# Kernel tuning notes

Measured on AMD Instinct MI355X. Metric: run time of the kernel, lower is better.

The kernel has to match this reference:

```python
import jax, jax.numpy as jnp
import numpy as np

T = 131072          # total characters across all words/sentences
N_WORDS = 32768
WORD_DIM = 1024
CHAR_DIM = 256
HIDDEN = 512
NUM_EMB = 40


def setup_inputs() -> dict:
    key = jax.random.key(0)
    ks = jax.random.split(key, 9)
    return {
        "word_emb": jax.random.normal(ks[0], (N_WORDS, WORD_DIM), jnp.float32),
        "char_ids": jax.random.randint(ks[1], (T,), 0, NUM_EMB, jnp.int32),
        "word_ids": jax.random.randint(ks[2], (T,), 0, N_WORDS, jnp.int32),
        "E": jax.random.normal(ks[3], (NUM_EMB, CHAR_DIM), jnp.float32),
        "W_ih": jax.random.normal(ks[4], (4 * HIDDEN, CHAR_DIM), jnp.float32) * 0.05,
        "b_ih": jax.random.normal(ks[5], (4 * HIDDEN,), jnp.float32) * 0.05,
        "b_hh": jax.random.normal(ks[6], (4 * HIDDEN,), jnp.float32) * 0.05,
        "W_lin": jax.random.normal(ks[7], (WORD_DIM, WORD_DIM + HIDDEN), jnp.float32) * 0.02,
        "b_lin": jax.random.normal(ks[8], (WORD_DIM,), jnp.float32) * 0.02,
    }


def reference(word_emb, char_ids, word_ids, E, W_ih, b_ih, b_hh, W_lin, b_lin):
    # Per-char embedding lookup: [T, CHAR_DIM]
    x = E[char_ids]
    # Single LSTM cell step from zero state (source runs LSTM with seq_len=1,
    # batch=num_chars; h0=c0=0 so W_hh @ h0 vanishes and only b_hh remains).
    gates = x @ W_ih.T + b_ih + b_hh            # [T, 4H], torch gate order i,f,g,o
    i, f, g, o = jnp.split(gates, 4, axis=-1)
    c = jax.nn.sigmoid(i) * jnp.tanh(g)          # f * c0 = 0
    h = jax.nn.sigmoid(o) * jnp.tanh(c)          # [T, HIDDEN]
    # Broadcast each word's embedding to its characters (torch .expand())
    we = word_emb[word_ids]                      # [T, WORD_DIM]
    combined = jnp.concatenate([we, h], axis=-1) # [T, WORD_DIM + HIDDEN]
    return jax.nn.relu(combined @ W_lin.T + b_lin)  # [T, WORD_DIM]
```

## Files before the change

kernel.cpp:

```cpp
#include <hip/hip_runtime.h>
#include <cstdint>
#include <cstddef>

#define T_TOTAL   131072
#define NWORDS    32768
#define WDIM      1024
#define CDIM      256
#define HID       512
#define NEMB      40
#define KDIM      1024
#define NDIM      1024

#define BM 128
#define BN 128
#define BK 32
#define NK (KDIM / BK)
#define EPS 132

#define NCONVB_BLKS (NDIM * KDIM / 4 / 256)
#define NCONVA_BLKS (NWORDS * KDIM / 4 / 256)

typedef __attribute__((ext_vector_type(8))) short bf16x8;
typedef __attribute__((ext_vector_type(4))) float f32x4;
typedef __attribute__((ext_vector_type(4))) unsigned short u16x4;

__device__ __forceinline__ unsigned short f2bf(float x) {
  union { float f; unsigned int u; } v; v.f = x;
  unsigned int r = v.u + 0x7fffu + ((v.u >> 16) & 1u);
  return (unsigned short)(r >> 16);
}
__device__ __forceinline__ float bf2f(unsigned short b) {
  union { float f; unsigned int u; } v; v.u = ((unsigned int)b) << 16;
  return v.f;
}

__device__ __forceinline__ void gld16(const void* src, void* lds) {
  __builtin_amdgcn_global_load_lds(
      (const __attribute__((address_space(1))) unsigned int*)src,
      (__attribute__((address_space(3))) unsigned int*)lds, 16, 0, 0);
}

template <bool DO_A>
__global__ __launch_bounds__(256) void k_prep(
    const float* __restrict__ word_emb, const float* __restrict__ E,
    const float* __restrict__ W_ih, const float* __restrict__ b_ih,
    const float* __restrict__ b_hh, const float* __restrict__ W_lin,
    const float* __restrict__ b_lin,
    unsigned short* __restrict__ Ah,
    unsigned short* __restrict__ Bh, unsigned short* __restrict__ Bl,
    float* __restrict__ Hc) {
  __shared__ float sx[CDIM];
  __shared__ float sh[HID];
  int b = blockIdx.x;
  int tid = threadIdx.x;

  if (b < NEMB) {
    int e = b;
    sx[tid] = E[e * CDIM + tid];
    __syncthreads();
    const float4* xv = (const float4*)sx;
#pragma unroll
    for (int rep = 0; rep < 2; ++rep) {
      int j = rep * 256 + tid;
      float si = b_ih[j] + b_hh[j];
      float sg = b_ih[1024 + j] + b_hh[1024 + j];
      float so = b_ih[1536 + j] + b_hh[1536 + j];
      const float4* wi = (const float4*)&W_ih[(size_t)j * CDIM];
      const float4* wg = (const float4*)&W_ih[(size_t)(1024 + j) * CDIM];
      const float4* wo = (const float4*)&W_ih[(size_t)(1536 + j) * CDIM];
      for (int k = 0; k < CDIM / 4; ++k) {
        float4 d = xv[k];
        float4 a = wi[k]; si += a.x*d.x + a.y*d.y + a.z*d.z + a.w*d.w;
        float4 g = wg[k]; sg += g.x*d.x + g.y*d.y + g.z*d.z + g.w*d.w;
        float4 c = wo[k]; so += c.x*d.x + c.y*d.y + c.z*d.z + c.w*d.w;
      }
      float iv = 1.f / (1.f + expf(-si));
      float cv = iv * tanhf(sg);
      float ov = 1.f / (1.f + expf(-so));
      sh[j] = ov * tanhf(cv);
    }
    __syncthreads();
    const float4* hv = (const float4*)sh;
#pragma unroll
    for (int rep = 0; rep < 4; ++rep) {
      int n = rep * 256 + tid;
      float s = b_lin[n];
      const float4* wl = (const float4*)&W_lin[(size_t)n * 1536 + 1024];
      for (int k = 0; k < HID / 4; ++k) {
        float4 a = wl[k], d = hv[k];
        s += a.x*d.x + a.y*d.y + a.z*d.z + a.w*d.w;
      }
      Hc[e * NDIM + n] = s;
    }
    return;
  }
  b -= NEMB;
  if (b < NCONVB_BLKS) {
    long idx = ((long)b * 256 + tid) * 4;
    long r = idx >> 10;
    int c = (int)(idx & 1023);
    const float4 v = *(const float4*)&W_lin[r * 1536 + c];
    unsigned short h0 = f2bf(v.x), h1 = f2bf(v.y), h2 = f2bf(v.z), h3 = f2bf(v.w);
    u16x4 H = {h0, h1, h2, h3};
    u16x4 L = {f2bf(v.x - bf2f(h0)), f2bf(v.y - bf2f(h1)),
               f2bf(v.z - bf2f(h2)), f2bf(v.w - bf2f(h3))};
    *(u16x4*)&Bh[idx] = H;
    *(u16x4*)&Bl[idx] = L;
    return;
  }
  if (DO_A) {
    b -= NCONVB_BLKS;
    long idx = ((long)b * 256 + tid) * 4;
    const float4 v = *(const float4*)&word_emb[idx];
    u16x4 H = {f2bf(v.x), f2bf(v.y), f2bf(v.z), f2bf(v.w)};
    *(u16x4*)&Ah[idx] = H;
  }
}

template <bool PRECONV>
__global__ __launch_bounds__(256, 3) void k_gemm_p(
    const float* __restrict__ Af,
    const unsigned short* __restrict__ Ah,
    const unsigned short* __restrict__ Bh, const unsigned short* __restrict__ Bl,
    float* __restrict__ P) {
  __shared__ __align__(16) char smem[PRECONV ? 49152 : 65536];

  int nwg = gridDim.x;
  int bid = blockIdx.x;
  int cpx = nwg >> 3;
  int swz = (bid & 7) * cpx + (bid >> 3);
  int bn = swz & 7;
  int bm = swz >> 3;

  int tid = threadIdx.x;
  int lane = tid & 63;
  int w = tid >> 6;
  int wr = w >> 1, wc = w & 1;
  int fr = lane & 15, fq = lane >> 4;

  size_t arow0 = (size_t)bm * BM;
  size_t brow0 = (size_t)bn * BN;

  f32x4 acc[4][4];
#pragma unroll
  for (int i = 0; i < 4; ++i)
#pragma unroll
    for (int j = 0; j < 4; ++j) acc[i][j] = (f32x4)0.0f;

  int bOff[4];
#pragma unroll
  for (int ni = 0; ni < 4; ++ni) {
    int row = wc * 64 + ni * 16 + fr;
    bOff[ni] = row * 64 + ((fq ^ ((row >> 1) & 3)) << 4);
  }
  size_t bS[2]; int bL[2];
#pragma unroll
  for (int is = 0; is < 2; ++is) {
    int off = is * 4096 + tid * 16;
    int r = off >> 6;
    int sp = (off >> 4) & 3;
    int colE = ((sp ^ ((r >> 1) & 3)) << 3);
    bS[is] = (brow0 + r) * KDIM + colE;
    bL[is] = is * 4096 + w * 1024;
  }
  int aOff[4];
#pragma unroll
  for (int mi = 0; mi < 4; ++mi) {
    int row = wr * 64 + mi * 16 + fr;
    aOff[mi] = row * 64 + ((fq ^ ((row >> 1) & 3)) << 4);
  }

  if (PRECONV) {
    size_t aS[2];
#pragma unroll
    for (int is = 0; is < 2; ++is) {
      int off = is * 4096 + tid * 16;
      int r = off >> 6;
      int sp = (off >> 4) & 3;
      int colE = ((sp ^ ((r >> 1) & 3)) << 3);
      aS[is] = (arow0 + r) * KDIM + colE;
    }

    auto STAGE = [&](int buf, int k0) {
      char* b = smem + buf * 24576;
#pragma unroll
      for (int is = 0; is < 2; ++is) {
        gld16(Ah + aS[is] + k0, b + bL[is]);
        gld16(Bh + bS[is] + k0, b + 8192 + bL[is]);
        gld16(Bl + bS[is] + k0, b + 16384 + bL[is]);
      }
    };

    STAGE(0, 0);
    for (int t = 0; t < NK; ++t) {
      char* bufc = smem + (t & 1) * 24576;
      if (t + 1 < NK) {
        STAGE((t + 1) & 1, (t + 1) * BK);
        asm volatile("s_waitcnt vmcnt(6)" ::: "memory");
      } else {
        asm volatile("s_waitcnt vmcnt(0)" ::: "memory");
      }
      __builtin_amdgcn_s_barrier();
      __builtin_amdgcn_sched_barrier(0);

      bf16x8 fah[4], fbh[4], fbl[4];
#pragma unroll
      for (int ni = 0; ni < 4; ++ni) {
        fbh[ni] = *(const bf16x8*)(bufc + 8192 + bOff[ni]);
        fbl[ni] = *(const bf16x8*)(bufc + 16384 + bOff[ni]);
      }
#pragma unroll
      for (int mi = 0; mi < 4; ++mi)
        fah[mi] = *(const bf16x8*)(bufc + aOff[mi]);
      __builtin_amdgcn_s_setprio(1);
#pragma unroll
      for (int mi = 0; mi < 4; ++mi)
#pragma unroll
        for (int ni = 0; ni < 4; ++ni) {
          acc[mi][ni] = __builtin_amdgcn_mfma_f32_16x16x32_bf16(fah[mi], fbh[ni], acc[mi][ni], 0, 0, 0);
          acc[mi][ni] = __builtin_amdgcn_mfma_f32_16x16x32_bf16(fah[mi], fbl[ni], acc[mi][ni], 0, 0, 0);
        }
      __builtin_amdgcn_s_setprio(0);
      __builtin_amdgcn_sched_barrier(0);
      __builtin_amdgcn_s_barrier();
    }
  } else {
    size_t aS[4]; int aL[4];
#pragma unroll
    for (int is = 0; is < 4; ++is) {
      int off = is * 4096 + tid * 16;
      int r = off >> 7;
      int sl = (off >> 4) & 7;
      int col = ((sl ^ (r & 7)) << 2);
      aS[is] = (arow0 + r) * KDIM + col;
      aL[is] = is * 4096 + w * 1024;
    }
    int a1[4], a2[4];
#pragma unroll
    for (int mi = 0; mi < 4; ++mi) {
      int row = wr * 64 + mi * 16 + fr;
      a1[mi] = row * 128 + (((fq << 1)     ^ (row & 7)) << 4);
      a2[mi] = row * 128 + (((fq << 1) + 1) ^ (row & 7)) * 16;
    }

    auto STAGE = [&](int buf, int k0) {
      char* b = smem + buf * 32768;
#pragma unroll
      for (int is = 0; is < 4; ++is) gld16(Af + aS[is] + k0, b + aL[is]);
#pragma unroll
      for (int is = 0; is < 2; ++is) {
        gld16(Bh + bS[is] + k0, b + 16384 + bL[is]);
        gld16(Bl + bS[is] + k0, b + 24576 + bL[is]);
      }
    };

    STAGE(0, 0);
    for (int t = 0; t < NK; ++t) {
      char* bufc = smem + (t & 1) * 32768;
      if (t + 1 < NK) {
        STAGE((t + 1) & 1, (t + 1) * BK);
        asm volatile("s_waitcnt vmcnt(8)" ::: "memory");
      } else {
        asm volatile("s_waitcnt vmcnt(0)" ::: "memory");
      }
      __builtin_amdgcn_s_barrier();
      __builtin_amdgcn_sched_barrier(0);

      bf16x8 fah[4], fbh[4], fbl[4];
#pragma unroll
      for (int ni = 0; ni < 4; ++ni) {
        fbh[ni] = *(const bf16x8*)(bufc + 16384 + bOff[ni]);
        fbl[ni] = *(const bf16x8*)(bufc + 24576 + bOff[ni]);
      }
#pragma unroll
      for (int mi = 0; mi < 4; ++mi) {
        float4 v1 = *(const float4*)(bufc + a1[mi]);
        float4 v2 = *(const float4*)(bufc + a2[mi]);
        union { bf16x8 v; unsigned short u[8]; } H;
        H.u[0] = f2bf(v1.x); H.u[1] = f2bf(v1.y); H.u[2] = f2bf(v1.z); H.u[3] = f2bf(v1.w);
        H.u[4] = f2bf(v2.x); H.u[5] = f2bf(v2.y); H.u[6] = f2bf(v2.z); H.u[7] = f2bf(v2.w);
        fah[mi] = H.v;
      }
      __builtin_amdgcn_s_setprio(1);
#pragma unroll
      for (int mi = 0; mi < 4; ++mi)
#pragma unroll
        for (int ni = 0; ni < 4; ++ni) {
          acc[mi][ni] = __builtin_amdgcn_mfma_f32_16x16x32_bf16(fah[mi], fbh[ni], acc[mi][ni], 0, 0, 0);
          acc[mi][ni] = __builtin_amdgcn_mfma_f32_16x16x32_bf16(fah[mi], fbl[ni], acc[mi][ni], 0, 0, 0);
        }
      __builtin_amdgcn_s_setprio(0);
      __builtin_amdgcn_sched_barrier(0);
      __builtin_amdgcn_s_barrier();
    }
  }

  float* ep = (float*)smem;
  __syncthreads();
#pragma unroll
  for (int half = 0; half < 2; ++half) {
    if (wr == half) {
#pragma unroll
      for (int mi = 0; mi < 4; ++mi)
#pragma unroll
        for (int ni = 0; ni < 4; ++ni)
#pragma unroll
          for (int j = 0; j < 4; ++j) {
            int r = mi * 16 + fq * 4 + j;
            int c = wc * 64 + ni * 16 + fr;
            ep[r * EPS + c] = acc[mi][ni][j];
          }
    }
    __syncthreads();
    for (int i = tid; i < 2048; i += 256) {
      int r = i >> 5;
      int c4 = (i & 31) << 2;
      float4 v = *(const float4*)&ep[r * EPS + c4];
      *(float4*)&P[(arow0 + half * 64 + r) * NDIM + brow0 + c4] = v;
    }
    __syncthreads();
  }
}

__global__ __launch_bounds__(256) void k_out(const int* __restrict__ wid,
                                             const int* __restrict__ cid,
                                             const float* __restrict__ P,
                                             const float* __restrict__ Hc,
                                             float* __restrict__ out) {
  int w = threadIdx.x >> 6, lane = threadIdx.x & 63;
  int t = blockIdx.x * 4 + w;
  int wd = wid[t], cd = cid[t];
  const f32x4* pr = (const f32x4*)&P[(size_t)wd << 10];
  const f32x4* hr = (const f32x4*)&Hc[(size_t)cd << 10];
  f32x4* orow = (f32x4*)&out[(size_t)t << 10];
#pragma unroll
  for (int ch = 0; ch < 4; ++ch) {
    int c = ch * 64 + lane;
    f32x4 a = pr[c];
    f32x4 h4 = hr[c];
    f32x4 r;
    r[0] = fmaxf(a[0] + h4[0], 0.f);
    r[1] = fmaxf(a[1] + h4[1], 0.f);
    r[2] = fmaxf(a[2] + h4[2], 0.f);
    r[3] = fmaxf(a[3] + h4[3], 0.f);
    __builtin_nontemporal_store(r, &orow[c]);
  }
}

extern "C" void kernel_launch(void* const* d_in, const int* in_sizes, int n_in,
                              void* d_out, int out_size, void* d_ws, size_t ws_size,
                              hipStream_t stream) {
  (void)in_sizes; (void)n_in; (void)out_size;
  const float* word_emb = (const float*)d_in[0];
  const int*   char_ids = (const int*)d_in[1];
  const int*   word_ids = (const int*)d_in[2];
  const float* E        = (const float*)d_in[3];
  const float* W_ih     = (const float*)d_in[4];
  const float* b_ih     = (const float*)d_in[5];
  const float* b_hh     = (const float*)d_in[6];
  const float* W_lin    = (const float*)d_in[7];
  const float* b_lin    = (const float*)d_in[8];
  float* out = (float*)d_out;
  char* ws = (char*)d_ws;

  size_t o = 0;
  auto alloc = [&](size_t b) { size_t r = o; o = (o + b + 255) & ~(size_t)255; return r; };
  size_t oHc = alloc((size_t)NEMB * NDIM * 4);
  size_t oBh = alloc((size_t)NDIM * KDIM * 2);
  size_t oBl = alloc((size_t)NDIM * KDIM * 2);
  size_t oP  = alloc((size_t)NWORDS * NDIM * 4);
  size_t szB = o;
  size_t oAh = alloc((size_t)NWORDS * KDIM * 2);
  size_t szA = o;

  float* Hc          = (float*)(ws + oHc);
  unsigned short* Bh = (unsigned short*)(ws + oBh);
  unsigned short* Bl = (unsigned short*)(ws + oBl);
  float* P           = (float*)(ws + oP);
  unsigned short* Ah = (unsigned short*)(ws + oAh);

  int grid = (NWORDS / BM) * (NDIM / BN);

  if (ws_size >= szA) {
    k_prep<true><<<NEMB + NCONVB_BLKS + NCONVA_BLKS, 256, 0, stream>>>(
        word_emb, E, W_ih, b_ih, b_hh, W_lin, b_lin, Ah, Bh, Bl, Hc);
    k_gemm_p<true><<<grid, 256, 0, stream>>>(word_emb, Ah, Bh, Bl, P);
  } else {
    k_prep<false><<<NEMB + NCONVB_BLKS, 256, 0, stream>>>(
        word_emb, E, W_ih, b_ih, b_hh, W_lin, b_lin, nullptr, Bh, Bl, Hc);
    k_gemm_p<false><<<grid, 256, 0, stream>>>(word_emb, nullptr, Bh, Bl, P);
  }
  k_out<<<T_TOTAL / 4, 256, 0, stream>>>(word_ids, char_ids, P, Hc, out);
}
```

Baseline: 414.0 us.

## Load A fragments directly from global into registers, bypassing LDS

In the preconverted GEMM path, each wave now loads its own A fragments from global memory straight into registers. These loads are double-buffered across iterations, and only the B hi/lo tiles are staged through shared memory. This cuts LDS traffic and the shared memory footprint (36 KB instead of 48 KB), which may allow more blocks per CU. The tradeoff is A reads that are not coalesced (strided 16-byte loads per lane), A data duplicated across the two wave columns, and more vector registers in use.

```diff
diff --git a/kernel.cpp b/kernel.cpp
--- a/kernel.cpp
+++ b/kernel.cpp
@@ -123,7 +123,7 @@
     const unsigned short* __restrict__ Ah,
     const unsigned short* __restrict__ Bh, const unsigned short* __restrict__ Bl,
     float* __restrict__ P) {
-  __shared__ __align__(16) char smem[PRECONV ? 49152 : 65536];
+  __shared__ __align__(16) char smem[PRECONV ? 36864 : 65536];
 
   int nwg = gridDim.x;
   int bid = blockIdx.x;
@@ -163,66 +163,60 @@
     bS[is] = (brow0 + r) * KDIM + colE;
     bL[is] = is * 4096 + w * 1024;
   }
-  int aOff[4];
-#pragma unroll
-  for (int mi = 0; mi < 4; ++mi) {
-    int row = wr * 64 + mi * 16 + fr;
-    aOff[mi] = row * 64 + ((fq ^ ((row >> 1) & 3)) << 4);
-  }
 
   if (PRECONV) {
-    size_t aS[2];
-#pragma unroll
-    for (int is = 0; is < 2; ++is) {
-      int off = is * 4096 + tid * 16;
-      int r = off >> 6;
-      int sp = (off >> 4) & 3;
-      int colE = ((sp ^ ((r >> 1) & 3)) << 3);
-      aS[is] = (arow0 + r) * KDIM + colE;
-    }
-
-    auto STAGE = [&](int buf, int k0) {
-      char* b = smem + buf * 24576;
+    size_t aBase = (arow0 + (size_t)(wr * 64 + fr)) * KDIM + fq * 8;
+
+    auto STAGE_B = [&](int buf, int k0) {
+      char* b = smem + buf * 16384;
 #pragma unroll
       for (int is = 0; is < 2; ++is) {
-        gld16(Ah + aS[is] + k0, b + bL[is]);
-        gld16(Bh + bS[is] + k0, b + 8192 + bL[is]);
-        gld16(Bl + bS[is] + k0, b + 16384 + bL[is]);
+        gld16(Bh + bS[is] + k0, b + bL[is]);
+        gld16(Bl + bS[is] + k0, b + 8192 + bL[is]);
       }
     };
-
-    STAGE(0, 0);
-    for (int t = 0; t < NK; ++t) {
-      char* bufc = smem + (t & 1) * 24576;
+    auto LOADA = [&](bf16x8 (&dst)[4], int k0) {
+#pragma unroll
+      for (int mi = 0; mi < 4; ++mi)
+        dst[mi] = *(const bf16x8*)(Ah + aBase + (size_t)(mi * 16) * KDIM + k0);
+    };
+    auto ITER = [&](int t, bf16x8 (&cur)[4], bf16x8 (&nxt)[4]) {
       if (t + 1 < NK) {
-        STAGE((t + 1) & 1, (t + 1) * BK);
-        asm volatile("s_waitcnt vmcnt(6)" ::: "memory");
+        STAGE_B((t + 1) & 1, (t + 1) * BK);
+        LOADA(nxt, (t + 1) * BK);
+        asm volatile("s_waitcnt vmcnt(8)" ::: "memory");
       } else {
         asm volatile("s_waitcnt vmcnt(0)" ::: "memory");
       }
       __builtin_amdgcn_s_barrier();
       __builtin_amdgcn_sched_barrier(0);
 
-      bf16x8 fah[4], fbh[4], fbl[4];
+      char* bufc = smem + (t & 1) * 16384;
+      bf16x8 fbh[4], fbl[4];
 #pragma unroll
       for (int ni = 0; ni < 4; ++ni) {
-        fbh[ni] = *(const bf16x8*)(bufc + 8192 + bOff[ni]);
-        fbl[ni] = *(const bf16x8*)(bufc + 16384 + bOff[ni]);
-      }
+        fbh[ni] = *(const bf16x8*)(bufc + bOff[ni]);
+        fbl[ni] = *(const bf16x8*)(bufc + 8192 + bOff[ni]);
+      }
+      __builtin_amdgcn_s_setprio(1);
 #pragma unroll
       for (int mi = 0; mi < 4; ++mi)
-        fah[mi] = *(const bf16x8*)(bufc + aOff[mi]);
-      __builtin_amdgcn_s_setprio(1);
-#pragma unroll
-      for (int mi = 0; mi < 4; ++mi)
 #pragma unroll
         for (int ni = 0; ni < 4; ++ni) {
-          acc[mi][ni] = __builtin_amdgcn_mfma_f32_16x16x32_bf16(fah[mi], fbh[ni], acc[mi][ni], 0, 0, 0);
-          acc[mi][ni] = __builtin_amdgcn_mfma_f32_16x16x32_bf16(fah[mi], fbl[ni], acc[mi][ni], 0, 0, 0);
+          acc[mi][ni] = __builtin_amdgcn_mfma_f32_16x16x32_bf16(cur[mi], fbh[ni], acc[mi][ni], 0, 0, 0);
+          acc[mi][ni] = __builtin_amdgcn_mfma_f32_16x16x32_bf16(cur[mi], fbl[ni], acc[mi][ni], 0, 0, 0);
         }
       __builtin_amdgcn_s_setprio(0);
       __builtin_amdgcn_sched_barrier(0);
       __builtin_amdgcn_s_barrier();
+    };
+
+    bf16x8 aA[4], aB[4];
+    STAGE_B(0, 0);
+    LOADA(aA, 0);
+    for (int t = 0; t < NK; t += 2) {
+      ITER(t, aA, aB);
+      ITER(t + 1, aB, aA);
     }
   } else {
     size_t aS[4]; int aL[4];
```

Result: slower. 454.6 us (+9.8%).

## Split hi/lo B passes into sequential K iterations to halve LDS staging

Applied to the files above, without the earlier changes.

The preconverted GEMM now runs 64 K-iterations: the first 32 use the bf16-high part of B and the next 32 use the low part, with A reloaded each time. Only one B tile is staged per step, so LDS per buffer drops from 24KB to 16KB, and launch bounds rise to 5 waves per SIMD to raise occupancy. The cost is that A is fetched from global memory twice, there are twice as many barriers, and the epilogue pad is removed, which may add LDS bank conflicts.

```diff
diff --git a/kernel.cpp b/kernel.cpp
--- a/kernel.cpp
+++ b/kernel.cpp
@@ -15,7 +15,7 @@
 #define BN 128
 #define BK 32
 #define NK (KDIM / BK)
-#define EPS 132
+#define NKV 64
 
 #define NCONVB_BLKS (NDIM * KDIM / 4 / 256)
 #define NCONVA_BLKS (NWORDS * KDIM / 4 / 256)
@@ -118,12 +118,13 @@
 }
 
 template <bool PRECONV>
-__global__ __launch_bounds__(256, 3) void k_gemm_p(
+__global__ __launch_bounds__(256, PRECONV ? 5 : 2) void k_gemm_p(
     const float* __restrict__ Af,
     const unsigned short* __restrict__ Ah,
     const unsigned short* __restrict__ Bh, const unsigned short* __restrict__ Bl,
     float* __restrict__ P) {
-  __shared__ __align__(16) char smem[PRECONV ? 49152 : 65536];
+  constexpr int EPSV = PRECONV ? 128 : 132;
+  __shared__ __align__(16) char smem[PRECONV ? 32768 : 65536];
 
   int nwg = gridDim.x;
   int bid = blockIdx.x;
@@ -181,34 +182,33 @@
       aS[is] = (arow0 + r) * KDIM + colE;
     }
 
-    auto STAGE = [&](int buf, int k0) {
-      char* b = smem + buf * 24576;
+    auto STAGE = [&](int buf, int t) {
+      char* b = smem + buf * 16384;
+      const unsigned short* Bsel = (t < 32) ? Bh : Bl;
+      int k0 = (t & 31) << 5;
 #pragma unroll
       for (int is = 0; is < 2; ++is) {
         gld16(Ah + aS[is] + k0, b + bL[is]);
-        gld16(Bh + bS[is] + k0, b + 8192 + bL[is]);
-        gld16(Bl + bS[is] + k0, b + 16384 + bL[is]);
+        gld16(Bsel + bS[is] + k0, b + 8192 + bL[is]);
       }
     };
 
     STAGE(0, 0);
-    for (int t = 0; t < NK; ++t) {
-      char* bufc = smem + (t & 1) * 24576;
-      if (t + 1 < NK) {
-        STAGE((t + 1) & 1, (t + 1) * BK);
-        asm volatile("s_waitcnt vmcnt(6)" ::: "memory");
+    for (int t = 0; t < NKV; ++t) {
+      char* bufc = smem + (t & 1) * 16384;
+      if (t + 1 < NKV) {
+        STAGE((t + 1) & 1, t + 1);
+        asm volatile("s_waitcnt vmcnt(4)" ::: "memory");
       } else {
         asm volatile("s_waitcnt vmcnt(0)" ::: "memory");
       }
       __builtin_amdgcn_s_barrier();
       __builtin_amdgcn_sched_barrier(0);
 
-      bf16x8 fah[4], fbh[4], fbl[4];
-#pragma unroll
-      for (int ni = 0; ni < 4; ++ni) {
-        fbh[ni] = *(const bf16x8*)(bufc + 8192 + bOff[ni]);
-        fbl[ni] = *(const bf16x8*)(bufc + 16384 + bOff[ni]);
-      }
+      bf16x8 fah[4], fb[4];
+#pragma unroll
+      for (int ni = 0; ni < 4; ++ni)
+        fb[ni] = *(const bf16x8*)(bufc + 8192 + bOff[ni]);
 #pragma unroll
       for (int mi = 0; mi < 4; ++mi)
         fah[mi] = *(const bf16x8*)(bufc + aOff[mi]);
@@ -216,10 +216,8 @@
 #pragma unroll
       for (int mi = 0; mi < 4; ++mi)
 #pragma unroll
-        for (int ni = 0; ni < 4; ++ni) {
-          acc[mi][ni] = __builtin_amdgcn_mfma_f32_16x16x32_bf16(fah[mi], fbh[ni], acc[mi][ni], 0, 0, 0);
-          acc[mi][ni] = __builtin_amdgcn_mfma_f32_16x16x32_bf16(fah[mi], fbl[ni], acc[mi][ni], 0, 0, 0);
-        }
+        for (int ni = 0; ni < 4; ++ni)
+          acc[mi][ni] = __builtin_amdgcn_mfma_f32_16x16x32_bf16(fah[mi], fb[ni], acc[mi][ni], 0, 0, 0);
       __builtin_amdgcn_s_setprio(0);
       __builtin_amdgcn_sched_barrier(0);
       __builtin_amdgcn_s_barrier();
@@ -308,14 +306,14 @@
           for (int j = 0; j < 4; ++j) {
             int r = mi * 16 + fq * 4 + j;
             int c = wc * 64 + ni * 16 + fr;
-            ep[r * EPS + c] = acc[mi][ni][j];
+            ep[r * EPSV + c] = acc[mi][ni][j];
           }
     }
     __syncthreads();
     for (int i = tid; i < 2048; i += 256) {
       int r = i >> 5;
       int c4 = (i & 31) << 2;
-      float4 v = *(const float4*)&ep[r * EPS + c4];
+      float4 v = *(const float4*)&ep[r * EPSV + c4];
       *(float4*)&P[(arow0 + half * 64 + r) * NDIM + brow0 + c4] = v;
     }
     __syncthreads();
```

New measurement: 702.3 us. 69.7% more time.
